# Kernel tuning notes

Hardware: AMD Instinct MI355X
Metric: run time of the kernel (lower is better)

## Reference

```python
import jax, jax.numpy as jnp
import numpy as np

N_NODES = 100000
N_EDGES = 1600000
IN_FEATS = 128
OUT_FEATS = 32
NEG_SLOPE = 0.2


def setup_inputs() -> dict:
    key = jax.random.key(0)
    k1, k2, k3, k4, k5 = jax.random.split(key, 5)
    h = jax.random.normal(k1, (N_NODES, IN_FEATS), dtype=jnp.float32)
    W = jax.random.normal(k2, (OUT_FEATS, IN_FEATS), dtype=jnp.float32) * 0.1
    a = jax.random.normal(k3, (1, 2 * OUT_FEATS), dtype=jnp.float32) * 0.1
    src = jax.random.randint(k4, (N_EDGES,), 0, N_NODES)
    dst = jax.random.randint(k5, (N_EDGES,), 0, N_NODES)
    return {"h": h, "W": W, "a": a, "src": src, "dst": dst}


def reference(h, W, a, src, dst):
    # feat dropout is identity in eval mode (feat_drop=0)
    z = h @ W.T                                   # [N, D] node projections
    # attention_func([z_src || z_dst]) = z_src @ a_l + z_dst @ a_r (no bias)
    a_l, a_r = a[0, :OUT_FEATS], a[0, OUT_FEATS:]
    el = z @ a_l                                  # [N]
    er = z @ a_r                                  # [N]
    e = jax.nn.leaky_relu(el[src] + er[dst], NEG_SLOPE)   # [E]
    # segment softmax over incoming edges per destination node
    e_max = jax.ops.segment_max(e, dst, num_segments=N_NODES)      # [N]
    e_max = jnp.where(jnp.isfinite(e_max), e_max, 0.0)             # empty segments
    ex = jnp.exp(e - e_max[dst])                                   # [E]
    denom = jax.ops.segment_sum(ex, dst, num_segments=N_NODES)     # [N]
    alpha = ex / jnp.maximum(denom[dst], 1e-16)                    # [E]
    # attn dropout identity in eval mode; weighted scatter-sum of messages
    msg = alpha[:, None] * z[src]                                  # [E, D]
    out = jax.ops.segment_sum(msg, dst, num_segments=N_NODES)      # [N, D]
    return out
```

## Files before the change

kernel.cpp:

```cpp
#include <hip/hip_runtime.h>
#include <hip/hip_bf16.h>

#define N_NODES_C  100000
#define N_EDGES_C  1600000
#define IN_FEATS_C 128
#define OUT_FEATS_C 32
#define NEG_SLOPE_C 0.2f

typedef __attribute__((ext_vector_type(8))) short short8;
typedef __attribute__((ext_vector_type(4))) float f32x4;

__device__ __hip_bfloat16 g_zb[N_NODES_C * OUT_FEATS_C];
__device__ float  g_el[N_NODES_C];
__device__ float  g_er[N_NODES_C];
__device__ int    g_head[N_NODES_C];
__device__ int2   g_ns[N_EDGES_C];
__device__ short8 g_wf_hi[2][4][64];
__device__ short8 g_wf_lo[2][4][64];

static __device__ __forceinline__ unsigned short f2bf(float x) {
    unsigned int u = __float_as_uint(x);
    unsigned int r = (u + 0x7FFFu + ((u >> 16) & 1u)) >> 16;
    return (unsigned short)r;
}
static __device__ __forceinline__ float bf2f(unsigned short h) {
    return __uint_as_float(((unsigned int)h) << 16);
}

__global__ __launch_bounds__(256) void k_prep(const float* __restrict__ W, int n_nodes, int nbn)
{
    int b = blockIdx.x;
    if (b < nbn) {
        int i = b * 256 + threadIdx.x;
        if (i < n_nodes) g_head[i] = -1;
        return;
    }
    int i = (b - nbn) * 256 + threadIdx.x;
    if (i >= 512) return;
    int lane = i & 63;
    int kt   = (i >> 6) & 3;
    int nt   = i >> 8;
    int row  = nt * 16 + (lane & 15);
    const float* p = W + (size_t)row * IN_FEATS_C + kt * 32 + (lane >> 4) * 8;
    float4 x0 = *(const float4*)(p);
    float4 x1 = *(const float4*)(p + 4);
    float xs[8] = {x0.x, x0.y, x0.z, x0.w, x1.x, x1.y, x1.z, x1.w};
    short8 hi, lo;
#pragma unroll
    for (int j = 0; j < 8; ++j) {
        unsigned short hb = f2bf(xs[j]);
        hi[j] = (short)hb;
        lo[j] = (short)f2bf(xs[j] - bf2f(hb));
    }
    g_wf_hi[nt][kt][lane] = hi;
    g_wf_lo[nt][kt][lane] = lo;
}

__global__ __launch_bounds__(256) void k_fat(const float* __restrict__ h,
                                             const float* __restrict__ a,
                                             const int* __restrict__ src,
                                             const int* __restrict__ dst,
                                             int n_nodes, int n_edges,
                                             int PB, int LB)
{
    int bid = blockIdx.x;
    if (bid % 5 == 0) {
        int pidx = bid / 5;
        if (pidx >= PB) return;
        int tile = pidx * 4 + (threadIdx.x >> 6);
        int ntiles = (n_nodes + 15) / 16;
        if (tile >= ntiles) return;
        int l   = threadIdx.x & 63;
        int r16 = l & 15;
        int g   = l >> 4;

        const float* hrow = h + (size_t)(tile * 16 + r16) * IN_FEATS_C + g * 8;
        f32x4 acc0 = {0.f, 0.f, 0.f, 0.f};
        f32x4 acc1 = {0.f, 0.f, 0.f, 0.f};

#pragma unroll
        for (int kt = 0; kt < 4; ++kt) {
            float4 x0 = *(const float4*)(hrow + kt * 32);
            float4 x1 = *(const float4*)(hrow + kt * 32 + 4);
            float xs[8] = {x0.x, x0.y, x0.z, x0.w, x1.x, x1.y, x1.z, x1.w};
            short8 ahi, alo;
#pragma unroll
            for (int j = 0; j < 8; ++j) {
                unsigned short hb = f2bf(xs[j]);
                ahi[j] = (short)hb;
                alo[j] = (short)f2bf(xs[j] - bf2f(hb));
            }
            short8 bh0 = g_wf_hi[0][kt][l], bl0 = g_wf_lo[0][kt][l];
            short8 bh1 = g_wf_hi[1][kt][l], bl1 = g_wf_lo[1][kt][l];
            acc0 = __builtin_amdgcn_mfma_f32_16x16x32_bf16(ahi, bh0, acc0, 0, 0, 0);
            acc0 = __builtin_amdgcn_mfma_f32_16x16x32_bf16(alo, bh0, acc0, 0, 0, 0);
            acc0 = __builtin_amdgcn_mfma_f32_16x16x32_bf16(ahi, bl0, acc0, 0, 0, 0);
            acc1 = __builtin_amdgcn_mfma_f32_16x16x32_bf16(ahi, bh1, acc1, 0, 0, 0);
            acc1 = __builtin_amdgcn_mfma_f32_16x16x32_bf16(alo, bh1, acc1, 0, 0, 0);
            acc1 = __builtin_amdgcn_mfma_f32_16x16x32_bf16(ahi, bl1, acc1, 0, 0, 0);
        }

        float al0 = a[r16], al1 = a[16 + r16];
        float ar0 = a[32 + r16], ar1 = a[48 + r16];
        float elp[4], erp[4];
        unsigned short* zb = (unsigned short*)g_zb;
#pragma unroll
        for (int r = 0; r < 4; ++r) {
            float z0 = acc0[r], z1 = acc1[r];
            int node = tile * 16 + g * 4 + r;
            zb[(size_t)node * OUT_FEATS_C + r16]      = f2bf(z0);
            zb[(size_t)node * OUT_FEATS_C + 16 + r16] = f2bf(z1);
            elp[r] = z0 * al0 + z1 * al1;
            erp[r] = z0 * ar0 + z1 * ar1;
        }
#pragma unroll
        for (int m = 1; m <= 8; m <<= 1) {
#pragma unroll
            for (int r = 0; r < 4; ++r) {
                elp[r] += __shfl_xor(elp[r], m, 64);
                erp[r] += __shfl_xor(erp[r], m, 64);
            }
        }
        int nodeb = tile * 16 + g * 4;
        if (r16 == 0) {
#pragma unroll
            for (int r = 0; r < 4; ++r) g_el[nodeb + r] = elp[r];
        } else if (r16 == 1) {
#pragma unroll
            for (int r = 0; r < 4; ++r) g_er[nodeb + r] = erp[r];
        }
    } else {
        int lidx = 4 * (bid / 5) + (bid % 5) - 1;
        if (lidx >= LB) return;
        int e = lidx * 256 + threadIdx.x;
        if (e < n_edges) {
            int nxt = atomicExch(&g_head[dst[e]], e);
            g_ns[e] = make_int2(nxt, src[e]);
        }
    }
}

__global__ __launch_bounds__(256) void k_gather(float* __restrict__ out, int n_nodes)
{
    int tid  = blockIdx.x * blockDim.x + threadIdx.x;
    int node = tid >> 5;
    int f    = tid & 31;
    if (node >= n_nodes) return;

    float er_d = g_er[node];
    const unsigned short* zb = (const unsigned short*)g_zb;
    float acc = 0.f, den = 0.f;

    int j = g_head[node];
    int2 ns = make_int2(-1, 0);
    if (j >= 0) ns = g_ns[j];
    while (j >= 0) {
        int jn = ns.x;
        int s  = ns.y;
        int2 ns2 = make_int2(-1, 0);
        if (jn >= 0) ns2 = g_ns[jn];
        float x = g_el[s] + er_d;
        x = (x > 0.f) ? x : NEG_SLOPE_C * x;
        float ex = __expf(x);
        float zf = bf2f(zb[(size_t)s * OUT_FEATS_C + f]);
        den += ex;
        acc = fmaf(ex, zf, acc);
        j = jn;
        ns = ns2;
    }
    out[(size_t)node * OUT_FEATS_C + f] = acc / fmaxf(den, 1e-16f);
}

extern "C" void kernel_launch(void* const* d_in, const int* in_sizes, int n_in,
                              void* d_out, int out_size, void* d_ws, size_t ws_size,
                              hipStream_t stream) {
    const float* h   = (const float*)d_in[0];
    const float* W   = (const float*)d_in[1];
    const float* a   = (const float*)d_in[2];
    const int*   src = (const int*)d_in[3];
    const int*   dst = (const int*)d_in[4];
    float* out = (float*)d_out;

    const int n_nodes = in_sizes[0] / IN_FEATS_C;
    const int n_edges = in_sizes[3];

    const int nbn    = (n_nodes + 255) / 256;
    const int ntiles = (n_nodes + 15) / 16;
    const int PB     = (ntiles + 3) / 4;
    const int LB     = (n_edges + 255) / 256;
    const int G      = 5 * ((PB > (LB + 3) / 4) ? PB : (LB + 3) / 4);

    k_prep<<<nbn + 2, 256, 0, stream>>>(W, n_nodes, nbn);
    k_fat<<<G, 256, 0, stream>>>(h, a, src, dst, n_nodes, n_edges, PB, LB);
    k_gather<<<(n_nodes * 32 + 255) / 256, 256, 0, stream>>>(out, n_nodes);
}
```

Before: 153.9 us.

## Split per-node edge lists into 8 chains and gather them in parallel

Edges are distributed across 8 separate linked-list heads per destination node, chosen by the low bits of the edge index. The gather kernel then gives each node a full 64-lane wavefront: 8 chains run concurrently, with 8 lanes per chain each loading 4 bf16 features. Partial sums are combined with cross-lane shuffles. The goal is to shorten the serial dependent pointer-chasing chain, at the cost of an 8x larger head array to initialize and twice as many gather threads.

```diff
diff --git a/kernel.cpp b/kernel.cpp
--- a/kernel.cpp
+++ b/kernel.cpp
@@ -6,6 +6,7 @@
 #define IN_FEATS_C 128
 #define OUT_FEATS_C 32
 #define NEG_SLOPE_C 0.2f
+#define NCH 8
 
 typedef __attribute__((ext_vector_type(8))) short short8;
 typedef __attribute__((ext_vector_type(4))) float f32x4;
@@ -13,7 +14,7 @@
 __device__ __hip_bfloat16 g_zb[N_NODES_C * OUT_FEATS_C];
 __device__ float  g_el[N_NODES_C];
 __device__ float  g_er[N_NODES_C];
-__device__ int    g_head[N_NODES_C];
+__device__ int    g_head[NCH][N_NODES_C];
 __device__ int2   g_ns[N_EDGES_C];
 __device__ short8 g_wf_hi[2][4][64];
 __device__ short8 g_wf_lo[2][4][64];
@@ -27,12 +28,12 @@
     return __uint_as_float(((unsigned int)h) << 16);
 }
 
-__global__ __launch_bounds__(256) void k_prep(const float* __restrict__ W, int n_nodes, int nbn)
+__global__ __launch_bounds__(256) void k_prep(const float* __restrict__ W, int nheads, int nbn)
 {
     int b = blockIdx.x;
     if (b < nbn) {
         int i = b * 256 + threadIdx.x;
-        if (i < n_nodes) g_head[i] = -1;
+        if (i < nheads) ((int*)g_head)[i] = -1;
         return;
     }
     int i = (b - nbn) * 256 + threadIdx.x;
@@ -134,7 +135,7 @@
         if (lidx >= LB) return;
         int e = lidx * 256 + threadIdx.x;
         if (e < n_edges) {
-            int nxt = atomicExch(&g_head[dst[e]], e);
+            int nxt = atomicExch(&g_head[e & (NCH - 1)][dst[e]], e);
             g_ns[e] = make_int2(nxt, src[e]);
         }
     }
@@ -143,15 +144,17 @@
 __global__ __launch_bounds__(256) void k_gather(float* __restrict__ out, int n_nodes)
 {
     int tid  = blockIdx.x * blockDim.x + threadIdx.x;
-    int node = tid >> 5;
-    int f    = tid & 31;
+    int node = tid >> 6;
     if (node >= n_nodes) return;
+    int l = threadIdx.x & 63;
+    int c = l >> 3;
+    int q = l & 7;
 
     float er_d = g_er[node];
     const unsigned short* zb = (const unsigned short*)g_zb;
-    float acc = 0.f, den = 0.f;
-
-    int j = g_head[node];
+    float a0 = 0.f, a1 = 0.f, a2 = 0.f, a3 = 0.f, den = 0.f;
+
+    int j = g_head[c][node];
     int2 ns = make_int2(-1, 0);
     if (j >= 0) ns = g_ns[j];
     while (j >= 0) {
@@ -162,13 +165,28 @@
         float x = g_el[s] + er_d;
         x = (x > 0.f) ? x : NEG_SLOPE_C * x;
         float ex = __expf(x);
-        float zf = bf2f(zb[(size_t)s * OUT_FEATS_C + f]);
+        ushort4 zv = *(const ushort4*)(zb + (size_t)s * OUT_FEATS_C + q * 4);
+        a0 = fmaf(ex, bf2f(zv.x), a0);
+        a1 = fmaf(ex, bf2f(zv.y), a1);
+        a2 = fmaf(ex, bf2f(zv.z), a2);
+        a3 = fmaf(ex, bf2f(zv.w), a3);
         den += ex;
-        acc = fmaf(ex, zf, acc);
         j = jn;
         ns = ns2;
     }
-    out[(size_t)node * OUT_FEATS_C + f] = acc / fmaxf(den, 1e-16f);
+#pragma unroll
+    for (int m = 8; m <= 32; m <<= 1) {
+        a0  += __shfl_xor(a0,  m, 64);
+        a1  += __shfl_xor(a1,  m, 64);
+        a2  += __shfl_xor(a2,  m, 64);
+        a3  += __shfl_xor(a3,  m, 64);
+        den += __shfl_xor(den, m, 64);
+    }
+    if (c == 0) {
+        float inv = 1.0f / fmaxf(den, 1e-16f);
+        float4 o = make_float4(a0 * inv, a1 * inv, a2 * inv, a3 * inv);
+        ((float4*)(out + (size_t)node * OUT_FEATS_C))[q] = o;
+    }
 }
 
 extern "C" void kernel_launch(void* const* d_in, const int* in_sizes, int n_in,
@@ -184,13 +202,14 @@
     const int n_nodes = in_sizes[0] / IN_FEATS_C;
     const int n_edges = in_sizes[3];
 
-    const int nbn    = (n_nodes + 255) / 256;
+    const int nheads = NCH * n_nodes;
+    const int nbn    = (nheads + 255) / 256;
     const int ntiles = (n_nodes + 15) / 16;
     const int PB     = (ntiles + 3) / 4;
     const int LB     = (n_edges + 255) / 256;
     const int G      = 5 * ((PB > (LB + 3) / 4) ? PB : (LB + 3) / 4);
 
-    k_prep<<<nbn + 2, 256, 0, stream>>>(W, n_nodes, nbn);
+    k_prep<<<nbn + 2, 256, 0, stream>>>(W, nheads, nbn);
     k_fat<<<G, 256, 0, stream>>>(h, a, src, dst, n_nodes, n_edges, PB, LB);
-    k_gather<<<(n_nodes * 32 + 255) / 256, 256, 0, stream>>>(out, n_nodes);
-}
+    k_gather<<<(n_nodes * 64 + 255) / 256, 256, 0, stream>>>(out, n_nodes);
+}
```

Measured after the change: 140.9 us. 8.4% less time.
